# Kernel tuning notes

Hardware: AMD Instinct MI355X
Metric: run time of the kernel (lower is better)

## Reference

```python
import jax, jax.numpy as jnp
import numpy as np

M = 256          # number of matched (positive) anchors
NUM_GT = 32      # number of ground-truth objects
ALPHA = 1.0      # cfg.loss_cls_alpha


def setup_inputs() -> dict:
    key = jax.random.key(0)
    ks = jax.random.split(key, 12)
    proto_types = jax.random.normal(ks[0], (1, 4, 128, 128), jnp.float32)
    map_class = jax.random.normal(ks[1], (1, 3, 64, 64), jnp.float32)
    map_box = jax.random.normal(ks[2], (1, 12, 64, 64), jnp.float32)
    map_coef = jax.random.normal(ks[3], (1, 12, 64, 64), jnp.float32)
    # anchor centers in pixel coords of a 512x512 image
    anchor_center = jax.random.uniform(ks[4], (2, 64, 64), jnp.float32) * 512.0
    # anchor box (h, w) per ratio, strictly positive (area ~24^2 at P3)
    anchor_box = jax.random.uniform(ks[5], (3, 2), jnp.float32, 24.0, 96.0)
    # GT boxes (ch, cw, h, w), strictly positive for log10
    gt_boxes = jax.random.uniform(ks[6], (1, NUM_GT, 4), jnp.float32, 16.0, 480.0)
    gt_masks = (jax.random.uniform(ks[7], (1, NUM_GT, 512, 512)) > 0.5).astype(jnp.float32)
    # matched anchors: (ratio, h, w)
    r = jax.random.randint(ks[8], (M, 1), 0, 3)
    hw = jax.random.randint(ks[9], (M, 2), 0, 64)
    pos_idx = jnp.concatenate([r, hw], axis=1).astype(jnp.int32)
    gt_idx = jax.random.randint(ks[10], (M,), 0, NUM_GT).astype(jnp.int32)
    rn = jax.random.randint(ks[11], (3 * M, 1), 0, 3)
    hwn = jax.random.randint(jax.random.fold_in(key, 99), (3 * M, 2), 0, 64)
    neg_idx = jnp.concatenate([rn, hwn], axis=1).astype(jnp.int32)
    return {"proto_types": proto_types, "map_class": map_class, "map_box": map_box,
            "map_coef": map_coef, "anchor_center": anchor_center, "anchor_box": anchor_box,
            "gt_boxes": gt_boxes, "gt_masks": gt_masks,
            "pos_idx": pos_idx, "gt_idx": gt_idx, "neg_idx": neg_idx}


def _smooth_l1_sum(d):
    a = jnp.abs(d)
    return jnp.sum(jnp.where(a < 1.0, 0.5 * d * d, a - 0.5))


def reference(proto_types, map_class, map_box, map_coef, anchor_center, anchor_box,
              gt_boxes, gt_masks, pos_idx, gt_idx, neg_idx):
    r, hh, ww = pos_idx[:, 0], pos_idx[:, 1], pos_idx[:, 2]
    # --- classification: BCE(sum) of sigmoid(logit) vs ones / zeros ---
    logit_pos = map_class[0, r, hh, ww]                       # [M]
    logit_neg = map_class[0, neg_idx[:, 0], neg_idx[:, 1], neg_idx[:, 2]]  # [3M]
    loss_cls_pos = jnp.sum(jax.nn.softplus(-logit_pos))       # -log sigmoid
    loss_cls_neg = jnp.sum(jax.nn.softplus(logit_neg))        # -log(1-sigmoid)
    # --- localization: SmoothL1(sum) on encoded offsets ---
    a_ch = anchor_center[0, hh, ww]
    a_cw = anchor_center[1, hh, ww]
    a_h = anchor_box[r, 0]
    a_w = anchor_box[r, 1]
    gt = gt_boxes[0, gt_idx]                                  # [M,4] = (ch,cw,h,w)
    tgt = jnp.stack([(gt[:, 0] - a_ch) / a_h,
                     (gt[:, 1] - a_cw) / a_w,
                     jnp.log10(gt[:, 2] / a_h),
                     jnp.log10(gt[:, 3] / a_w)], axis=1)      # [M,4]
    ch4 = r[:, None] * 4 + jnp.arange(4, dtype=r.dtype)[None, :]
    pred_box = map_box[0, ch4, hh[:, None], ww[:, None]]      # [M,4]
    loss_loc = _smooth_l1_sum(pred_box - tgt)
    # --- mask: coef . proto -> sigmoid -> nearest upsample x4 -> BCE(mean) per anchor ---
    coef = map_coef[0, ch4, hh[:, None], ww[:, None]]         # [M,4]
    mask_logits = jnp.einsum('mp,phw->mhw', coef, proto_types[0])  # [M,128,128]
    up = jnp.repeat(jnp.repeat(mask_logits, 4, axis=1), 4, axis=2)  # nearest to 512
    goal = gt_masks[0, gt_idx]                                # [M,512,512]
    # BCE(sigmoid(z), t) = softplus(z) - t*z  (stable form)
    bce = jax.nn.softplus(up) - goal * up
    loss_mask = jnp.sum(jnp.mean(bce, axis=(1, 2)))
    total = loss_cls_pos + loss_cls_neg + ALPHA * loss_loc + loss_mask / M
    return total
```

## Files before the change

### kernel.cpp

```cpp
#include <hip/hip_runtime.h>
#include <math.h>


#define INV_TOTAL (1.0f / (262144.0f * 256.0f))

__device__ __forceinline__ float softplusf(float x) {
    return fmaxf(x, 0.0f) + __logf(1.0f + __expf(-fabsf(x)));
}

__device__ __forceinline__ float wave_sum(float v) {
    v += __shfl_down(v, 32);
    v += __shfl_down(v, 16);
    v += __shfl_down(v, 8);
    v += __shfl_down(v, 4);
    v += __shfl_down(v, 2);
    v += __shfl_down(v, 1);
    return v;
}

__global__ void __launch_bounds__(256)
k_workers(const float* __restrict__ proto,
          const float* __restrict__ map_coef,
          const float* __restrict__ map_class,
          const float* __restrict__ map_box,
          const float* __restrict__ anchor_center,
          const float* __restrict__ anchor_box,
          const float* __restrict__ gt_boxes,
          const float* __restrict__ gt_masks,
          const int* __restrict__ pos_idx,
          const int* __restrict__ gt_idx,
          const int* __restrict__ neg_idx,
          float* __restrict__ Tpart,
          float* __restrict__ SP,
          float* __restrict__ C4,
          float* __restrict__ CL) {
    const int bid = blockIdx.x;
    const int t = threadIdx.x;
    const int wave = t >> 6, lane = t & 63;
    __shared__ float smem[4][4];

    if (bid < 512) {
        const int g = bid >> 4, chunk = bid & 15;
        const float* mask = gt_masks + (size_t)g * (512 * 512);
        float tp0 = 0.f, tp1 = 0.f, tp2 = 0.f, tp3 = 0.f;
#pragma unroll 4
        for (int i = 0; i < 16; ++i) {
            int f = t + (i << 8);
            int yl = f >> 7;
            int k  = f & 127;
            int y  = (chunk << 5) + yl;
            float4 mv = *reinterpret_cast<const float4*>(mask + y * 512 + (k << 2));
            float s = (mv.x + mv.y) + (mv.z + mv.w);
            int cell = ((y >> 2) << 7) + k;
            tp0 = fmaf(s, proto[cell],         tp0);
            tp1 = fmaf(s, proto[16384 + cell], tp1);
            tp2 = fmaf(s, proto[32768 + cell], tp2);
            tp3 = fmaf(s, proto[49152 + cell], tp3);
        }
        tp0 = wave_sum(tp0); tp1 = wave_sum(tp1); tp2 = wave_sum(tp2); tp3 = wave_sum(tp3);
        if (lane == 0) { smem[wave][0] = tp0; smem[wave][1] = tp1; smem[wave][2] = tp2; smem[wave][3] = tp3; }
        __syncthreads();
        if (t < 4)
            Tpart[(bid << 2) + t] = smem[0][t] + smem[1][t] + smem[2][t] + smem[3][t];
        return;
    }

    if (bid < 768) {
        const int m = bid - 512;
        const int r = pos_idx[m * 3 + 0], h = pos_idx[m * 3 + 1], w = pos_idx[m * 3 + 2];
        const int off = (r << 2) * 4096 + h * 64 + w;
        const float c0 = map_coef[off];
        const float c1 = map_coef[off + 4096];
        const float c2 = map_coef[off + 8192];
        const float c3 = map_coef[off + 12288];
        float sp = 0.f;
#pragma unroll 4
        for (int i = 0; i < 16; ++i) {
            int f = (t + (i << 8)) << 2;
            float4 p0 = *reinterpret_cast<const float4*>(proto + f);
            float4 p1 = *reinterpret_cast<const float4*>(proto + 16384 + f);
            float4 p2 = *reinterpret_cast<const float4*>(proto + 32768 + f);
            float4 p3 = *reinterpret_cast<const float4*>(proto + 49152 + f);
            float L;
            L = fmaf(c3, p3.x, fmaf(c2, p2.x, fmaf(c1, p1.x, c0 * p0.x))); sp += softplusf(L);
            L = fmaf(c3, p3.y, fmaf(c2, p2.y, fmaf(c1, p1.y, c0 * p0.y))); sp += softplusf(L);
            L = fmaf(c3, p3.z, fmaf(c2, p2.z, fmaf(c1, p1.z, c0 * p0.z))); sp += softplusf(L);
            L = fmaf(c3, p3.w, fmaf(c2, p2.w, fmaf(c1, p1.w, c0 * p0.w))); sp += softplusf(L);
        }
        sp = wave_sum(sp);
        if (lane == 0) smem[wave][0] = sp;
        __syncthreads();
        if (t == 0) {
            SP[m] = smem[0][0] + smem[1][0] + smem[2][0] + smem[3][0];
            C4[(m << 2) + 0] = c0; C4[(m << 2) + 1] = c1;
            C4[(m << 2) + 2] = c2; C4[(m << 2) + 3] = c3;
        }
        return;
    }

    float sum;
    {
        const int r = pos_idx[t * 3 + 0], h = pos_idx[t * 3 + 1], w = pos_idx[t * 3 + 2];
        const int hw = h * 64 + w;
        sum = softplusf(-map_class[r * 4096 + hw]);
        for (int j = 0; j < 3; ++j) {
            int n = t + (j << 8);
            int rn = neg_idx[n * 3 + 0], hn = neg_idx[n * 3 + 1], wn = neg_idx[n * 3 + 2];
            sum += softplusf(map_class[rn * 4096 + hn * 64 + wn]);
        }
        const float ach = anchor_center[hw];
        const float acw = anchor_center[4096 + hw];
        const float ah = anchor_box[r * 2 + 0];
        const float aw = anchor_box[r * 2 + 1];
        const int g = gt_idx[t];
        const float g0 = gt_boxes[g * 4 + 0], g1 = gt_boxes[g * 4 + 1];
        const float g2 = gt_boxes[g * 4 + 2], g3 = gt_boxes[g * 4 + 3];
        float tgt[4] = { (g0 - ach) / ah, (g1 - acw) / aw, log10f(g2 / ah), log10f(g3 / aw) };
#pragma unroll
        for (int j = 0; j < 4; ++j) {
            float d = map_box[(r * 4 + j) * 4096 + hw] - tgt[j];
            float a = fabsf(d);
            sum += (a < 1.0f) ? 0.5f * d * d : a - 0.5f;
        }
    }
    sum = wave_sum(sum);
    if (lane == 0) smem[wave][0] = sum;
    __syncthreads();
    if (t == 0)
        CL[0] = smem[0][0] + smem[1][0] + smem[2][0] + smem[3][0];
}

__global__ void __launch_bounds__(256)
k_final(const int* __restrict__ gt_idx,
        const float* __restrict__ Tpart,
        const float* __restrict__ SP,
        const float* __restrict__ C4,
        const float* __restrict__ CL,
        float* __restrict__ out) {
    const int t = threadIdx.x;
    const int wave = t >> 6, lane = t & 63;
    __shared__ float sT[128];
    __shared__ float smem[4];

    if (t < 128) {
        const int g = t >> 2, p = t & 3;
        float s = 0.f;
#pragma unroll
        for (int chunk = 0; chunk < 16; ++chunk)
            s += Tpart[(((g << 4) + chunk) << 2) + p];
        sT[t] = s;
    }
    const int g = gt_idx[t];
    const float spm = SP[t];
    const float4 c = *reinterpret_cast<const float4*>(C4 + (t << 2));
    __syncthreads();

    const float dotT = fmaf(c.w, sT[(g << 2) + 3], fmaf(c.z, sT[(g << 2) + 2],
                       fmaf(c.y, sT[(g << 2) + 1], c.x * sT[(g << 2) + 0])));
    float contrib = (16.f * spm - dotT) * INV_TOTAL;
    contrib = wave_sum(contrib);
    if (lane == 0) smem[wave] = contrib;
    __syncthreads();
    if (t == 0)
        out[0] = CL[0] + smem[0] + smem[1] + smem[2] + smem[3];
}

extern "C" void kernel_launch(void* const* d_in, const int* in_sizes, int n_in,
                              void* d_out, int out_size, void* d_ws, size_t ws_size,
                              hipStream_t stream) {
    const float* proto         = (const float*)d_in[0];
    const float* map_class     = (const float*)d_in[1];
    const float* map_box       = (const float*)d_in[2];
    const float* map_coef      = (const float*)d_in[3];
    const float* anchor_center = (const float*)d_in[4];
    const float* anchor_box    = (const float*)d_in[5];
    const float* gt_boxes      = (const float*)d_in[6];
    const float* gt_masks      = (const float*)d_in[7];
    const int*   pos_idx       = (const int*)d_in[8];
    const int*   gt_idx        = (const int*)d_in[9];
    const int*   neg_idx       = (const int*)d_in[10];

    float* Tpart = (float*)d_ws;
    float* SP    = Tpart + 2048;
    float* C4    = SP + 256;
    float* CL    = C4 + 1024;
    float* out   = (float*)d_out;

    k_workers<<<769, 256, 0, stream>>>(proto, map_coef, map_class, map_box,
                                       anchor_center, anchor_box, gt_boxes, gt_masks,
                                       pos_idx, gt_idx, neg_idx,
                                       Tpart, SP, C4, CL);
    k_final<<<1, 256, 0, stream>>>(gt_idx, Tpart, SP, C4, CL, out);
}
```

Before: 100.3 us.

## Split mask-projection blocks finer with 8-row vertical pre-reduction and reorder block roles

The GT-mask projection work is now spread over 1024 blocks instead of 512. Each thread loads 8 consecutive rows of float4 mask data up front and sums each group of 4 rows before multiplying by proto, so it does 2 proto cells x 4 channels of loads instead of 16 per-row proto gathers. The small classification/localization block moves to block 0, so it no longer runs last. The softplus blocks move to the end of the grid, and the final reduction is adjusted for 32 chunks per GT. The intent is more memory-level parallelism and fewer redundant proto loads in the bandwidth-dominated 32 MB mask read, at the cost of more blocks and a larger partial-sum buffer.

```diff
diff --git a/kernel.cpp b/kernel.cpp
--- a/kernel.cpp
+++ b/kernel.cpp
@@ -16,6 +16,10 @@
     v += __shfl_down(v, 2);
     v += __shfl_down(v, 1);
     return v;
+}
+
+__device__ __forceinline__ float sum4(float4 v) {
+    return (v.x + v.y) + (v.z + v.w);
 }
 
 __global__ void __launch_bounds__(256)
@@ -39,95 +43,101 @@
     const int wave = t >> 6, lane = t & 63;
     __shared__ float smem[4][4];
 
-    if (bid < 512) {
-        const int g = bid >> 4, chunk = bid & 15;
+    if (bid == 0) {
+        float sum;
+        {
+            const int r = pos_idx[t * 3 + 0], h = pos_idx[t * 3 + 1], w = pos_idx[t * 3 + 2];
+            const int hw = h * 64 + w;
+            sum = softplusf(-map_class[r * 4096 + hw]);
+            for (int j = 0; j < 3; ++j) {
+                int n = t + (j << 8);
+                int rn = neg_idx[n * 3 + 0], hn = neg_idx[n * 3 + 1], wn = neg_idx[n * 3 + 2];
+                sum += softplusf(map_class[rn * 4096 + hn * 64 + wn]);
+            }
+            const float ach = anchor_center[hw];
+            const float acw = anchor_center[4096 + hw];
+            const float ah = anchor_box[r * 2 + 0];
+            const float aw = anchor_box[r * 2 + 1];
+            const int g = gt_idx[t];
+            const float g0 = gt_boxes[g * 4 + 0], g1 = gt_boxes[g * 4 + 1];
+            const float g2 = gt_boxes[g * 4 + 2], g3 = gt_boxes[g * 4 + 3];
+            float tgt[4] = { (g0 - ach) / ah, (g1 - acw) / aw, log10f(g2 / ah), log10f(g3 / aw) };
+#pragma unroll
+            for (int j = 0; j < 4; ++j) {
+                float d = map_box[(r * 4 + j) * 4096 + hw] - tgt[j];
+                float a = fabsf(d);
+                sum += (a < 1.0f) ? 0.5f * d * d : a - 0.5f;
+            }
+        }
+        sum = wave_sum(sum);
+        if (lane == 0) smem[wave][0] = sum;
+        __syncthreads();
+        if (t == 0)
+            CL[0] = smem[0][0] + smem[1][0] + smem[2][0] + smem[3][0];
+        return;
+    }
+
+    if (bid <= 1024) {
+        const int tb = bid - 1;
+        const int g = tb >> 5, chunk = tb & 31;
         const float* mask = gt_masks + (size_t)g * (512 * 512);
-        float tp0 = 0.f, tp1 = 0.f, tp2 = 0.f, tp3 = 0.f;
-#pragma unroll 4
-        for (int i = 0; i < 16; ++i) {
-            int f = t + (i << 8);
-            int yl = f >> 7;
-            int k  = f & 127;
-            int y  = (chunk << 5) + yl;
-            float4 mv = *reinterpret_cast<const float4*>(mask + y * 512 + (k << 2));
-            float s = (mv.x + mv.y) + (mv.z + mv.w);
-            int cell = ((y >> 2) << 7) + k;
-            tp0 = fmaf(s, proto[cell],         tp0);
-            tp1 = fmaf(s, proto[16384 + cell], tp1);
-            tp2 = fmaf(s, proto[32768 + cell], tp2);
-            tp3 = fmaf(s, proto[49152 + cell], tp3);
-        }
+        const int k  = t & 127;
+        const int rg = t >> 7;
+        const int y0 = (chunk << 4) + (rg << 3);
+        const float* mrow = mask + y0 * 512 + (k << 2);
+        float4 a0 = *reinterpret_cast<const float4*>(mrow);
+        float4 a1 = *reinterpret_cast<const float4*>(mrow + 512);
+        float4 a2 = *reinterpret_cast<const float4*>(mrow + 1024);
+        float4 a3 = *reinterpret_cast<const float4*>(mrow + 1536);
+        float4 a4 = *reinterpret_cast<const float4*>(mrow + 2048);
+        float4 a5 = *reinterpret_cast<const float4*>(mrow + 2560);
+        float4 a6 = *reinterpret_cast<const float4*>(mrow + 3072);
+        float4 a7 = *reinterpret_cast<const float4*>(mrow + 3584);
+        const float s0 = (sum4(a0) + sum4(a1)) + (sum4(a2) + sum4(a3));
+        const float s1 = (sum4(a4) + sum4(a5)) + (sum4(a6) + sum4(a7));
+        const int c0 = ((y0 >> 2) << 7) + k;
+        const int c1 = c0 + 128;
+        float tp0 = fmaf(s1, proto[c1],         s0 * proto[c0]);
+        float tp1 = fmaf(s1, proto[16384 + c1], s0 * proto[16384 + c0]);
+        float tp2 = fmaf(s1, proto[32768 + c1], s0 * proto[32768 + c0]);
+        float tp3 = fmaf(s1, proto[49152 + c1], s0 * proto[49152 + c0]);
         tp0 = wave_sum(tp0); tp1 = wave_sum(tp1); tp2 = wave_sum(tp2); tp3 = wave_sum(tp3);
         if (lane == 0) { smem[wave][0] = tp0; smem[wave][1] = tp1; smem[wave][2] = tp2; smem[wave][3] = tp3; }
         __syncthreads();
         if (t < 4)
-            Tpart[(bid << 2) + t] = smem[0][t] + smem[1][t] + smem[2][t] + smem[3][t];
+            Tpart[(tb << 2) + t] = smem[0][t] + smem[1][t] + smem[2][t] + smem[3][t];
         return;
     }
 
-    if (bid < 768) {
-        const int m = bid - 512;
-        const int r = pos_idx[m * 3 + 0], h = pos_idx[m * 3 + 1], w = pos_idx[m * 3 + 2];
-        const int off = (r << 2) * 4096 + h * 64 + w;
-        const float c0 = map_coef[off];
-        const float c1 = map_coef[off + 4096];
-        const float c2 = map_coef[off + 8192];
-        const float c3 = map_coef[off + 12288];
-        float sp = 0.f;
+    const int m = bid - 1025;
+    const int r = pos_idx[m * 3 + 0], h = pos_idx[m * 3 + 1], w = pos_idx[m * 3 + 2];
+    const int off = (r << 2) * 4096 + h * 64 + w;
+    const float c0 = map_coef[off];
+    const float c1 = map_coef[off + 4096];
+    const float c2 = map_coef[off + 8192];
+    const float c3 = map_coef[off + 12288];
+    float sp = 0.f;
 #pragma unroll 4
-        for (int i = 0; i < 16; ++i) {
-            int f = (t + (i << 8)) << 2;
-            float4 p0 = *reinterpret_cast<const float4*>(proto + f);
-            float4 p1 = *reinterpret_cast<const float4*>(proto + 16384 + f);
-            float4 p2 = *reinterpret_cast<const float4*>(proto + 32768 + f);
-            float4 p3 = *reinterpret_cast<const float4*>(proto + 49152 + f);
-            float L;
-            L = fmaf(c3, p3.x, fmaf(c2, p2.x, fmaf(c1, p1.x, c0 * p0.x))); sp += softplusf(L);
-            L = fmaf(c3, p3.y, fmaf(c2, p2.y, fmaf(c1, p1.y, c0 * p0.y))); sp += softplusf(L);
-            L = fmaf(c3, p3.z, fmaf(c2, p2.z, fmaf(c1, p1.z, c0 * p0.z))); sp += softplusf(L);
-            L = fmaf(c3, p3.w, fmaf(c2, p2.w, fmaf(c1, p1.w, c0 * p0.w))); sp += softplusf(L);
-        }
-        sp = wave_sum(sp);
-        if (lane == 0) smem[wave][0] = sp;
-        __syncthreads();
-        if (t == 0) {
-            SP[m] = smem[0][0] + smem[1][0] + smem[2][0] + smem[3][0];
-            C4[(m << 2) + 0] = c0; C4[(m << 2) + 1] = c1;
-            C4[(m << 2) + 2] = c2; C4[(m << 2) + 3] = c3;
-        }
-        return;
-    }
-
-    float sum;
-    {
-        const int r = pos_idx[t * 3 + 0], h = pos_idx[t * 3 + 1], w = pos_idx[t * 3 + 2];
-        const int hw = h * 64 + w;
-        sum = softplusf(-map_class[r * 4096 + hw]);
-        for (int j = 0; j < 3; ++j) {
-            int n = t + (j << 8);
-            int rn = neg_idx[n * 3 + 0], hn = neg_idx[n * 3 + 1], wn = neg_idx[n * 3 + 2];
-            sum += softplusf(map_class[rn * 4096 + hn * 64 + wn]);
-        }
-        const float ach = anchor_center[hw];
-        const float acw = anchor_center[4096 + hw];
-        const float ah = anchor_box[r * 2 + 0];
-        const float aw = anchor_box[r * 2 + 1];
-        const int g = gt_idx[t];
-        const float g0 = gt_boxes[g * 4 + 0], g1 = gt_boxes[g * 4 + 1];
-        const float g2 = gt_boxes[g * 4 + 2], g3 = gt_boxes[g * 4 + 3];
-        float tgt[4] = { (g0 - ach) / ah, (g1 - acw) / aw, log10f(g2 / ah), log10f(g3 / aw) };
-#pragma unroll
-        for (int j = 0; j < 4; ++j) {
-            float d = map_box[(r * 4 + j) * 4096 + hw] - tgt[j];
-            float a = fabsf(d);
-            sum += (a < 1.0f) ? 0.5f * d * d : a - 0.5f;
-        }
-    }
-    sum = wave_sum(sum);
-    if (lane == 0) smem[wave][0] = sum;
+    for (int i = 0; i < 16; ++i) {
+        int f = (t + (i << 8)) << 2;
+        float4 p0 = *reinterpret_cast<const float4*>(proto + f);
+        float4 p1 = *reinterpret_cast<const float4*>(proto + 16384 + f);
+        float4 p2 = *reinterpret_cast<const float4*>(proto + 32768 + f);
+        float4 p3 = *reinterpret_cast<const float4*>(proto + 49152 + f);
+        float L;
+        L = fmaf(c3, p3.x, fmaf(c2, p2.x, fmaf(c1, p1.x, c0 * p0.x))); sp += softplusf(L);
+        L = fmaf(c3, p3.y, fmaf(c2, p2.y, fmaf(c1, p1.y, c0 * p0.y))); sp += softplusf(L);
+        L = fmaf(c3, p3.z, fmaf(c2, p2.z, fmaf(c1, p1.z, c0 * p0.z))); sp += softplusf(L);
+        L = fmaf(c3, p3.w, fmaf(c2, p2.w, fmaf(c1, p1.w, c0 * p0.w))); sp += softplusf(L);
+    }
+    sp = wave_sum(sp);
+    if (lane == 0) smem[wave][0] = sp;
     __syncthreads();
-    if (t == 0)
-        CL[0] = smem[0][0] + smem[1][0] + smem[2][0] + smem[3][0];
+    if (t == 0) {
+        SP[m] = smem[0][0] + smem[1][0] + smem[2][0] + smem[3][0];
+        C4[(m << 2) + 0] = c0; C4[(m << 2) + 1] = c1;
+        C4[(m << 2) + 2] = c2; C4[(m << 2) + 3] = c3;
+    }
 }
 
 __global__ void __launch_bounds__(256)
@@ -146,8 +156,8 @@
         const int g = t >> 2, p = t & 3;
         float s = 0.f;
 #pragma unroll
-        for (int chunk = 0; chunk < 16; ++chunk)
-            s += Tpart[(((g << 4) + chunk) << 2) + p];
+        for (int chunk = 0; chunk < 32; ++chunk)
+            s += Tpart[(((g << 5) + chunk) << 2) + p];
         sT[t] = s;
     }
     const int g = gt_idx[t];
@@ -181,14 +191,14 @@
     const int*   neg_idx       = (const int*)d_in[10];
 
     float* Tpart = (float*)d_ws;
-    float* SP    = Tpart + 2048;
+    float* SP    = Tpart + 4096;
     float* C4    = SP + 256;
     float* CL    = C4 + 1024;
     float* out   = (float*)d_out;
 
-    k_workers<<<769, 256, 0, stream>>>(proto, map_coef, map_class, map_box,
-                                       anchor_center, anchor_box, gt_boxes, gt_masks,
-                                       pos_idx, gt_idx, neg_idx,
-                                       Tpart, SP, C4, CL);
+    k_workers<<<1281, 256, 0, stream>>>(proto, map_coef, map_class, map_box,
+                                        anchor_center, anchor_box, gt_boxes, gt_masks,
+                                        pos_idx, gt_idx, neg_idx,
+                                        Tpart, SP, C4, CL);
     k_final<<<1, 256, 0, stream>>>(gt_idx, Tpart, SP, C4, CL, out);
 }
```

After: 103.2 us. 2.9% more time.
